# Kernel tuning notes

Measured on AMD Instinct MI355X. Metric: run time of the kernel, lower is better.

The kernel has to match this reference:

```python
import jax, jax.numpy as jnp
import numpy as np

N, E, IN, HID, CLS = 40000, 640000, 128, 256, 40
K = 2  # SGConv k hops

def setup_inputs() -> dict:
    key = jax.random.key(0)
    ks = jax.random.split(key, 5)
    features = jax.random.normal(ks[0], (N, IN), dtype=jnp.float32)
    src = jax.random.randint(ks[1], (E,), 0, N)
    dst = jax.random.randint(ks[2], (E,), 0, N)
    # SGConv fc: in_feats -> n_hidden
    W1 = jax.random.normal(ks[3], (IN, HID), dtype=jnp.float32) / np.float32(np.sqrt(IN))
    b1 = jnp.zeros((HID,), dtype=jnp.float32)
    # model-level linear: n_hidden -> n_classes
    W2 = jax.random.normal(ks[4], (HID, CLS), dtype=jnp.float32) / np.float32(np.sqrt(HID))
    b2 = jnp.zeros((CLS,), dtype=jnp.float32)
    return {"features": features, "src": src, "dst": dst,
            "W1": W1, "b1": b1, "W2": W2, "b2": b2}

def reference(features, src, dst, W1, b1, W2, b2):
    # symmetric degree norm (DGL SGConv: in-degree, clamp min=1)
    deg = jax.ops.segment_sum(jnp.ones((E,), jnp.float32), dst, num_segments=N)
    norm = jax.lax.rsqrt(jnp.maximum(deg, 1.0))[:, None]  # [N,1]
    h = features
    for _ in range(K):
        h = h * norm
        h = jax.ops.segment_sum(h[src], dst, num_segments=N)  # A @ h via edge scatter
        h = h * norm
    h = h @ W1 + b1            # SGConv fc
    return jax.nn.relu(h) @ W2 + b2  # model relu + linear
```

## Files before the change

### kernel.cpp

```cpp
#include <hip/hip_runtime.h>

#define N_NODES 40000
#define N_EDGES 640000
#define IN_F 128
#define HID_F 256
#define CLS_F 40
#define CLS_P 48
#define MB 32
#define TS_LD 264
#define A_LD 136

typedef __attribute__((ext_vector_type(8))) short bf16x8;
typedef __attribute__((ext_vector_type(4))) float f32x4;
typedef __attribute__((ext_vector_type(4))) _Float16 half4;
typedef __attribute__((ext_vector_type(8))) _Float16 half8;

#define MFMA(a, b, c) __builtin_amdgcn_mfma_f32_16x16x32_bf16(a, b, c, 0, 0, 0)

__device__ __forceinline__ unsigned short f32_to_bf16_rne(float f) {
    unsigned int u = __float_as_uint(f);
    unsigned int r = u + 0x7fffu + ((u >> 16) & 1u);
    return (unsigned short)(r >> 16);
}

__device__ __forceinline__ int aswz(int row, int col_us) {
    return row * A_LD + (col_us ^ ((row & 7) << 3));
}


__global__ void k_count(const int* __restrict__ dst, int* __restrict__ counts) {
    int e = blockIdx.x * blockDim.x + threadIdx.x;
    if (e < N_EDGES) atomicAdd(&counts[dst[e]], 1);
}

__global__ void k_scan1(const int* __restrict__ counts, int* __restrict__ bsum) {
    __shared__ int s[256];
    int i = blockIdx.x * 256 + threadIdx.x;
    s[threadIdx.x] = (i < N_NODES) ? counts[i] : 0;
    __syncthreads();
    for (int off = 128; off > 0; off >>= 1) {
        if (threadIdx.x < off) s[threadIdx.x] += s[threadIdx.x + off];
        __syncthreads();
    }
    if (threadIdx.x == 0) bsum[blockIdx.x] = s[0];
}

__global__ void k_scan2(int* __restrict__ bsum, int nb) {
    __shared__ int s[256];
    int t = threadIdx.x;
    int v = (t < nb) ? bsum[t] : 0;
    s[t] = v;
    __syncthreads();
    for (int off = 1; off < 256; off <<= 1) {
        int x = (t >= off) ? s[t - off] : 0;
        __syncthreads();
        s[t] += x;
        __syncthreads();
    }
    if (t < nb) bsum[t] = s[t] - v;
}

__global__ void k_scan3n(const int* __restrict__ counts, const int* __restrict__ bsum,
                         int* __restrict__ rowptr, int* __restrict__ cursor,
                         float* __restrict__ norm, float* __restrict__ norm2) {
    __shared__ int s[256];
    int t = threadIdx.x;
    int i = blockIdx.x * 256 + t;
    int v = (i < N_NODES) ? counts[i] : 0;
    s[t] = v;
    __syncthreads();
    for (int off = 1; off < 256; off <<= 1) {
        int x = (t >= off) ? s[t - off] : 0;
        __syncthreads();
        s[t] += x;
        __syncthreads();
    }
    if (i < N_NODES) {
        int excl = s[t] - v + bsum[blockIdx.x];
        rowptr[i] = excl;
        cursor[i] = excl;
        float d = (float)v;
        float r = rsqrtf(fmaxf(d, 1.0f));
        norm[i] = r;
        norm2[i] = r * r;
    }
}


__global__ __launch_bounds__(256) void k_fsp(
        const int* __restrict__ src, const int* __restrict__ dst,
        int* __restrict__ cursor, unsigned short* __restrict__ csr_src,
        const float* __restrict__ features, const float* __restrict__ norm,
        _Float16* __restrict__ xs,
        const float* __restrict__ W1, const float* __restrict__ W2,
        unsigned short* __restrict__ w1hi, unsigned short* __restrict__ w1lo,
        unsigned short* __restrict__ w2hi, unsigned short* __restrict__ w2lo) {
    int b = blockIdx.x;
    if (b < 2500) {
        int e = b * 256 + threadIdx.x;
        int d = dst[e];
        int p = atomicAdd(&cursor[d], 1);
        csr_src[p] = (unsigned short)src[e];
    } else if (b < 5000) {
        int i = (b - 2500) * 256 + threadIdx.x;
        float s = norm[i >> 4];
        float4 a = ((const float4*)features)[i * 2];
        float4 c = ((const float4*)features)[i * 2 + 1];
        half8 h;
        h[0] = (_Float16)(a.x * s); h[1] = (_Float16)(a.y * s);
        h[2] = (_Float16)(a.z * s); h[3] = (_Float16)(a.w * s);
        h[4] = (_Float16)(c.x * s); h[5] = (_Float16)(c.y * s);
        h[6] = (_Float16)(c.z * s); h[7] = (_Float16)(c.w * s);
        ((half8*)xs)[i] = h;
    } else {
        int idx = (b - 5000) * 256 + threadIdx.x;
        if (idx < IN_F * HID_F) {
            int k = idx >> 8;
            int c = idx & 255;
            float v = W1[idx];
            unsigned short hi = f32_to_bf16_rne(v);
            float fh = __uint_as_float((unsigned)hi << 16);
            w1hi[c * IN_F + k] = hi;
            w1lo[c * IN_F + k] = f32_to_bf16_rne(v - fh);
        }
        int idx2 = idx - IN_F * HID_F;
        if (idx2 >= 0 && idx2 < CLS_P * HID_F) {
            int c = idx2 >> 8;
            int k = idx2 & 255;
            float v = (c < CLS_F) ? W2[k * CLS_F + c] : 0.f;
            unsigned short hi = f32_to_bf16_rne(v);
            float fh = __uint_as_float((unsigned)hi << 16);
            w2hi[c * HID_F + k] = hi;
            w2lo[c * HID_F + k] = f32_to_bf16_rne(v - fh);
        }
    }
}


__global__ __launch_bounds__(256) void k_hop(
        const _Float16* __restrict__ gin, _Float16* __restrict__ gout,
        const unsigned short* __restrict__ csr_src, const int* __restrict__ rowptr,
        const int* __restrict__ counts, const float* __restrict__ oscale) {
    int gid  = blockIdx.x * 8 + (threadIdx.x >> 5);
    int lane = threadIdx.x & 31;
    if (gid >= N_NODES) return;
    int start = rowptr[gid];
    int cnt   = counts[gid];
    const _Float16* base = gin + lane * 4;
    float4 acc = make_float4(0.f, 0.f, 0.f, 0.f);
    int i = 0;
    for (; i + 3 < cnt; i += 4) {
        int s0 = csr_src[start + i];     int s1 = csr_src[start + i + 1];
        int s2 = csr_src[start + i + 2]; int s3 = csr_src[start + i + 3];
        half4 v0 = *(const half4*)(base + (size_t)s0 * IN_F);
        half4 v1 = *(const half4*)(base + (size_t)s1 * IN_F);
        half4 v2 = *(const half4*)(base + (size_t)s2 * IN_F);
        half4 v3 = *(const half4*)(base + (size_t)s3 * IN_F);
        acc.x += (float)v0[0] + (float)v1[0] + (float)v2[0] + (float)v3[0];
        acc.y += (float)v0[1] + (float)v1[1] + (float)v2[1] + (float)v3[1];
        acc.z += (float)v0[2] + (float)v1[2] + (float)v2[2] + (float)v3[2];
        acc.w += (float)v0[3] + (float)v1[3] + (float)v2[3] + (float)v3[3];
    }
    for (; i < cnt; i++) {
        int s = csr_src[start + i];
        half4 v = *(const half4*)(base + (size_t)s * IN_F);
        acc.x += (float)v[0]; acc.y += (float)v[1];
        acc.z += (float)v[2]; acc.w += (float)v[3];
    }
    float sc = oscale[gid];
    half4 o;
    o[0] = (_Float16)(acc.x * sc); o[1] = (_Float16)(acc.y * sc);
    o[2] = (_Float16)(acc.z * sc); o[3] = (_Float16)(acc.w * sc);
    *(half4*)(gout + (size_t)gid * IN_F + lane * 4) = o;
}


__global__ __launch_bounds__(256, 2) void k_mlp(
        const _Float16* __restrict__ h1,
        const unsigned short* __restrict__ csr_src, const int* __restrict__ rowptr,
        const int* __restrict__ counts, const float* __restrict__ norm,
        const unsigned short* __restrict__ w1hi, const unsigned short* __restrict__ w1lo,
        const float* __restrict__ b1,
        const unsigned short* __restrict__ w2hi, const unsigned short* __restrict__ w2lo,
        const float* __restrict__ b2,
        float* __restrict__ out) {
    __shared__ __align__(16) unsigned short ahi[MB * A_LD];
    __shared__ __align__(16) unsigned short alo[MB * A_LD];
    __shared__ __align__(16) unsigned short tshi[MB * TS_LD];
    __shared__ __align__(16) unsigned short tslo[MB * TS_LD];
    int n0 = blockIdx.x * MB;
    int t  = threadIdx.x;
    int w  = t >> 6;
    int l  = t & 63;
    int lr = l & 15;
    int lg = l >> 4;

    bf16x8 b1h[4][4], b1l[4][4];
    float  b1v[4];
    #pragma unroll
    for (int ct = 0; ct < 4; ct++) {
        int col = w * 64 + ct * 16 + lr;
        const unsigned short* bhp = w1hi + (size_t)col * IN_F + lg * 8;
        const unsigned short* blp = w1lo + (size_t)col * IN_F + lg * 8;
        #pragma unroll
        for (int kq = 0; kq < 4; kq++) {
            b1h[ct][kq] = *(const bf16x8*)(bhp + kq * 32);
            b1l[ct][kq] = *(const bf16x8*)(blp + kq * 32);
        }
        b1v[ct] = b1[col];
    }

    {
        int grp  = t >> 5;
        int lane = t & 31;
        for (int nn = grp; nn < MB; nn += 8) {
            int gid = n0 + nn;
            int start = rowptr[gid];
            int cnt   = counts[gid];
            const _Float16* base = h1 + lane * 4;
            float4 acc = make_float4(0.f, 0.f, 0.f, 0.f);
            int i = 0;
            for (; i + 3 < cnt; i += 4) {
                int s0 = csr_src[start + i];     int s1 = csr_src[start + i + 1];
                int s2 = csr_src[start + i + 2]; int s3 = csr_src[start + i + 3];
                half4 v0 = *(const half4*)(base + (size_t)s0 * IN_F);
                half4 v1 = *(const half4*)(base + (size_t)s1 * IN_F);
                half4 v2 = *(const half4*)(base + (size_t)s2 * IN_F);
                half4 v3 = *(const half4*)(base + (size_t)s3 * IN_F);
                acc.x += (float)v0[0] + (float)v1[0] + (float)v2[0] + (float)v3[0];
                acc.y += (float)v0[1] + (float)v1[1] + (float)v2[1] + (float)v3[1];
                acc.z += (float)v0[2] + (float)v1[2] + (float)v2[2] + (float)v3[2];
                acc.w += (float)v0[3] + (float)v1[3] + (float)v2[3] + (float)v3[3];
            }
            for (; i < cnt; i++) {
                int s = csr_src[start + i];
                half4 v = *(const half4*)(base + (size_t)s * IN_F);
                acc.x += (float)v[0]; acc.y += (float)v[1];
                acc.z += (float)v[2]; acc.w += (float)v[3];
            }
            float sc = norm[gid];
            float vv[4] = {acc.x * sc, acc.y * sc, acc.z * sc, acc.w * sc};
            ushort4 h, lo4;
            unsigned short* hp = (unsigned short*)&h;
            unsigned short* lp = (unsigned short*)&lo4;
            #pragma unroll
            for (int j = 0; j < 4; j++) {
                unsigned short hi = f32_to_bf16_rne(vv[j]);
                float fh = __uint_as_float((unsigned)hi << 16);
                hp[j] = hi;
                lp[j] = f32_to_bf16_rne(vv[j] - fh);
            }
            int o = aswz(nn, lane * 4);
            *(ushort4*)&ahi[o] = h;
            *(ushort4*)&alo[o] = lo4;
        }
    }
    __syncthreads();

    #pragma unroll
    for (int rt = 0; rt < 2; rt++) {
        bf16x8 aH[4], aL[4];
        #pragma unroll
        for (int kq = 0; kq < 4; kq++) {
            int o = aswz(rt * 16 + lr, (kq * 4 + lg) * 8);
            aH[kq] = *(const bf16x8*)&ahi[o];
            aL[kq] = *(const bf16x8*)&alo[o];
        }
        #pragma unroll
        for (int ct = 0; ct < 4; ct++) {
            f32x4 acc = {0.f, 0.f, 0.f, 0.f};
            #pragma unroll
            for (int kq = 0; kq < 4; kq++) {
                acc = MFMA(aH[kq], b1h[ct][kq], acc);
                acc = MFMA(aH[kq], b1l[ct][kq], acc);
                acc = MFMA(aL[kq], b1h[ct][kq], acc);
            }
            int col = w * 64 + ct * 16 + lr;
            #pragma unroll
            for (int r = 0; r < 4; r++) {
                int row = rt * 16 + lg * 4 + r;
                float v = acc[r] + b1v[ct];
                v = v > 0.f ? v : 0.f;
                unsigned short hi = f32_to_bf16_rne(v);
                float fh = __uint_as_float((unsigned)hi << 16);
                tshi[row * TS_LD + col] = hi;
                tslo[row * TS_LD + col] = f32_to_bf16_rne(v - fh);
            }
        }
    }
    __syncthreads();

    if (w < 3) {
        int col = w * 16 + lr;
        bf16x8 b2h[8], b2l[8];
        const unsigned short* bhp = w2hi + (size_t)col * HID_F + lg * 8;
        const unsigned short* blp = w2lo + (size_t)col * HID_F + lg * 8;
        #pragma unroll
        for (int kk = 0; kk < 8; kk++) {
            b2h[kk] = *(const bf16x8*)(bhp + kk * 32);
            b2l[kk] = *(const bf16x8*)(blp + kk * 32);
        }
        float bias = (col < CLS_F) ? b2[col] : 0.f;
        #pragma unroll
        for (int rt2 = 0; rt2 < 2; rt2++) {
            const unsigned short* ahp = tshi + (rt2 * 16 + lr) * TS_LD + lg * 8;
            const unsigned short* alp = tslo + (rt2 * 16 + lr) * TS_LD + lg * 8;
            f32x4 acc0 = {0.f, 0.f, 0.f, 0.f};
            f32x4 acc1 = {0.f, 0.f, 0.f, 0.f};
            #pragma unroll
            for (int kk = 0; kk < 4; kk++) {
                bf16x8 a_h0 = *(const bf16x8*)(ahp + kk * 32);
                bf16x8 a_l0 = *(const bf16x8*)(alp + kk * 32);
                bf16x8 a_h1 = *(const bf16x8*)(ahp + (kk + 4) * 32);
                bf16x8 a_l1 = *(const bf16x8*)(alp + (kk + 4) * 32);
                acc0 = MFMA(a_h0, b2h[kk], acc0);
                acc1 = MFMA(a_h1, b2h[kk + 4], acc1);
                acc0 = MFMA(a_h0, b2l[kk], acc0);
                acc1 = MFMA(a_h1, b2l[kk + 4], acc1);
                acc0 = MFMA(a_l0, b2h[kk], acc0);
                acc1 = MFMA(a_l1, b2h[kk + 4], acc1);
            }
            if (col < CLS_F) {
                #pragma unroll
                for (int r = 0; r < 4; r++) {
                    int mrow = n0 + rt2 * 16 + lg * 4 + r;
                    out[(size_t)mrow * CLS_F + col] = acc0[r] + acc1[r] + bias;
                }
            }
        }
    }
}


extern "C" void kernel_launch(void* const* d_in, const int* in_sizes, int n_in,
                              void* d_out, int out_size, void* d_ws, size_t ws_size,
                              hipStream_t stream) {
    const float* features = (const float*)d_in[0];
    const int*   src      = (const int*)d_in[1];
    const int*   dst      = (const int*)d_in[2];
    const float* W1       = (const float*)d_in[3];
    const float* b1       = (const float*)d_in[4];
    const float* W2       = (const float*)d_in[5];
    const float* b2       = (const float*)d_in[6];
    float*       out      = (float*)d_out;

    char* ws = (char*)d_ws;
    size_t off = 0;
    auto alloc = [&](size_t bytes) -> void* {
        void* p = ws + off;
        off += (bytes + 255) & ~(size_t)255;
        return p;
    };
    int*   counts = (int*)alloc((size_t)N_NODES * 4);
    int*   rowptr = (int*)alloc((size_t)N_NODES * 4);
    int*   cursor = (int*)alloc((size_t)N_NODES * 4);
    int*   bsum   = (int*)alloc(256 * 4);
    float* norm   = (float*)alloc((size_t)N_NODES * 4);
    float* norm2  = (float*)alloc((size_t)N_NODES * 4);
    unsigned short* csr = (unsigned short*)alloc((size_t)N_EDGES * 2);
    _Float16* xs  = (_Float16*)alloc((size_t)N_NODES * IN_F * 2);
    _Float16* h1  = (_Float16*)alloc((size_t)N_NODES * IN_F * 2);
    unsigned short* w1hi = (unsigned short*)alloc((size_t)HID_F * IN_F * 2);
    unsigned short* w1lo = (unsigned short*)alloc((size_t)HID_F * IN_F * 2);
    unsigned short* w2hi = (unsigned short*)alloc((size_t)CLS_P * HID_F * 2);
    unsigned short* w2lo = (unsigned short*)alloc((size_t)CLS_P * HID_F * 2);

    hipMemsetAsync(counts, 0, (size_t)N_NODES * 4, stream);

    int nb = (N_NODES + 255) / 256;
    k_count<<<(N_EDGES + 255) / 256, 256, 0, stream>>>(dst, counts);
    k_scan1<<<nb, 256, 0, stream>>>(counts, bsum);
    k_scan2<<<1, 256, 0, stream>>>(bsum, nb);
    k_scan3n<<<nb, 256, 0, stream>>>(counts, bsum, rowptr, cursor, norm, norm2);

    int prep_blocks = (IN_F * HID_F + CLS_P * HID_F + 255) / 256;
    k_fsp<<<5000 + prep_blocks, 256, 0, stream>>>(
        src, dst, cursor, csr, features, norm, xs, W1, W2, w1hi, w1lo, w2hi, w2lo);

    k_hop<<<(N_NODES + 7) / 8, 256, 0, stream>>>(xs, h1, csr, rowptr, counts, norm2);
    k_mlp<<<N_NODES / MB, 256, 0, stream>>>(h1, csr, rowptr, counts, norm,
                                            w1hi, w1lo, b1, w2hi, w2lo, b2, out);
}
```

Before: 262.5 us.

## Switch MLP to fp16 hi/lo MFMA, split second hop out, single-pass scan

Measured after the change: 222.9 us. 15.1% less time.

```diff
diff --git a/kernel.cpp b/kernel.cpp
--- a/kernel.cpp
+++ b/kernel.cpp
@@ -8,62 +8,29 @@
 #define CLS_P 48
 #define MB 32
 #define TS_LD 264
-#define A_LD 136
-
-typedef __attribute__((ext_vector_type(8))) short bf16x8;
+#define LO_SCALE 2048.0f
+#define LO_INV   4.8828125e-4f
+
+typedef __attribute__((ext_vector_type(8))) _Float16 f16x8;
 typedef __attribute__((ext_vector_type(4))) float f32x4;
 typedef __attribute__((ext_vector_type(4))) _Float16 half4;
 typedef __attribute__((ext_vector_type(8))) _Float16 half8;
 
-#define MFMA(a, b, c) __builtin_amdgcn_mfma_f32_16x16x32_bf16(a, b, c, 0, 0, 0)
-
-__device__ __forceinline__ unsigned short f32_to_bf16_rne(float f) {
-    unsigned int u = __float_as_uint(f);
-    unsigned int r = u + 0x7fffu + ((u >> 16) & 1u);
-    return (unsigned short)(r >> 16);
-}
-
-__device__ __forceinline__ int aswz(int row, int col_us) {
-    return row * A_LD + (col_us ^ ((row & 7) << 3));
-}
-
-
-__global__ void k_count(const int* __restrict__ dst, int* __restrict__ counts) {
+#define MFMA16(a, b, c) __builtin_amdgcn_mfma_f32_16x16x32_f16(a, b, c, 0, 0, 0)
+
+
+__global__ void k_count(const int* __restrict__ dst, int* __restrict__ counts,
+                        int* __restrict__ gcur) {
     int e = blockIdx.x * blockDim.x + threadIdx.x;
+    if (e == 0) *gcur = 0;
     if (e < N_EDGES) atomicAdd(&counts[dst[e]], 1);
 }
 
-__global__ void k_scan1(const int* __restrict__ counts, int* __restrict__ bsum) {
+__global__ void k_scanA(const int* __restrict__ counts, int* __restrict__ gcur,
+                        int* __restrict__ rowptr, int* __restrict__ cursor,
+                        float* __restrict__ norm, float* __restrict__ norm2) {
     __shared__ int s[256];
-    int i = blockIdx.x * 256 + threadIdx.x;
-    s[threadIdx.x] = (i < N_NODES) ? counts[i] : 0;
-    __syncthreads();
-    for (int off = 128; off > 0; off >>= 1) {
-        if (threadIdx.x < off) s[threadIdx.x] += s[threadIdx.x + off];
-        __syncthreads();
-    }
-    if (threadIdx.x == 0) bsum[blockIdx.x] = s[0];
-}
-
-__global__ void k_scan2(int* __restrict__ bsum, int nb) {
-    __shared__ int s[256];
-    int t = threadIdx.x;
-    int v = (t < nb) ? bsum[t] : 0;
-    s[t] = v;
-    __syncthreads();
-    for (int off = 1; off < 256; off <<= 1) {
-        int x = (t >= off) ? s[t - off] : 0;
-        __syncthreads();
-        s[t] += x;
-        __syncthreads();
-    }
-    if (t < nb) bsum[t] = s[t] - v;
-}
-
-__global__ void k_scan3n(const int* __restrict__ counts, const int* __restrict__ bsum,
-                         int* __restrict__ rowptr, int* __restrict__ cursor,
-                         float* __restrict__ norm, float* __restrict__ norm2) {
-    __shared__ int s[256];
+    __shared__ int base;
     int t = threadIdx.x;
     int i = blockIdx.x * 256 + t;
     int v = (i < N_NODES) ? counts[i] : 0;
@@ -75,12 +42,13 @@
         s[t] += x;
         __syncthreads();
     }
+    if (t == 255) base = atomicAdd(gcur, s[255]);
+    __syncthreads();
     if (i < N_NODES) {
-        int excl = s[t] - v + bsum[blockIdx.x];
+        int excl = base + s[t] - v;
         rowptr[i] = excl;
         cursor[i] = excl;
-        float d = (float)v;
-        float r = rsqrtf(fmaxf(d, 1.0f));
+        float r = rsqrtf(fmaxf((float)v, 1.0f));
         norm[i] = r;
         norm2[i] = r * r;
     }
@@ -93,8 +61,8 @@
         const float* __restrict__ features, const float* __restrict__ norm,
         _Float16* __restrict__ xs,
         const float* __restrict__ W1, const float* __restrict__ W2,
-        unsigned short* __restrict__ w1hi, unsigned short* __restrict__ w1lo,
-        unsigned short* __restrict__ w2hi, unsigned short* __restrict__ w2lo) {
+        _Float16* __restrict__ w1hi, _Float16* __restrict__ w1lo,
+        _Float16* __restrict__ w2hi, _Float16* __restrict__ w2lo) {
     int b = blockIdx.x;
     if (b < 2500) {
         int e = b * 256 + threadIdx.x;
@@ -118,20 +86,18 @@
             int k = idx >> 8;
             int c = idx & 255;
             float v = W1[idx];
-            unsigned short hi = f32_to_bf16_rne(v);
-            float fh = __uint_as_float((unsigned)hi << 16);
+            _Float16 hi = (_Float16)v;
             w1hi[c * IN_F + k] = hi;
-            w1lo[c * IN_F + k] = f32_to_bf16_rne(v - fh);
+            w1lo[c * IN_F + k] = (_Float16)((v - (float)hi) * LO_SCALE);
         }
         int idx2 = idx - IN_F * HID_F;
         if (idx2 >= 0 && idx2 < CLS_P * HID_F) {
             int c = idx2 >> 8;
             int k = idx2 & 255;
             float v = (c < CLS_F) ? W2[k * CLS_F + c] : 0.f;
-            unsigned short hi = f32_to_bf16_rne(v);
-            float fh = __uint_as_float((unsigned)hi << 16);
+            _Float16 hi = (_Float16)v;
             w2hi[c * HID_F + k] = hi;
-            w2lo[c * HID_F + k] = f32_to_bf16_rne(v - fh);
+            w2lo[c * HID_F + k] = (_Float16)((v - (float)hi) * LO_SCALE);
         }
     }
 }
@@ -176,18 +142,13 @@
 
 
 __global__ __launch_bounds__(256, 2) void k_mlp(
-        const _Float16* __restrict__ h1,
-        const unsigned short* __restrict__ csr_src, const int* __restrict__ rowptr,
-        const int* __restrict__ counts, const float* __restrict__ norm,
-        const unsigned short* __restrict__ w1hi, const unsigned short* __restrict__ w1lo,
+        const _Float16* __restrict__ h2,
+        const _Float16* __restrict__ w1hi, const _Float16* __restrict__ w1lo,
         const float* __restrict__ b1,
-        const unsigned short* __restrict__ w2hi, const unsigned short* __restrict__ w2lo,
+        const _Float16* __restrict__ w2hi, const _Float16* __restrict__ w2lo,
         const float* __restrict__ b2,
         float* __restrict__ out) {
-    __shared__ __align__(16) unsigned short ahi[MB * A_LD];
-    __shared__ __align__(16) unsigned short alo[MB * A_LD];
-    __shared__ __align__(16) unsigned short tshi[MB * TS_LD];
-    __shared__ __align__(16) unsigned short tslo[MB * TS_LD];
+    __shared__ __align__(16) _Float16 ts[MB * TS_LD];
     int n0 = blockIdx.x * MB;
     int t  = threadIdx.x;
     int w  = t >> 6;
@@ -195,96 +156,49 @@
     int lr = l & 15;
     int lg = l >> 4;
 
-    bf16x8 b1h[4][4], b1l[4][4];
-    float  b1v[4];
+    f16x8 b1h[4][4], b1l[4][4];
+    float b1v[4];
     #pragma unroll
     for (int ct = 0; ct < 4; ct++) {
         int col = w * 64 + ct * 16 + lr;
-        const unsigned short* bhp = w1hi + (size_t)col * IN_F + lg * 8;
-        const unsigned short* blp = w1lo + (size_t)col * IN_F + lg * 8;
+        const _Float16* bhp = w1hi + (size_t)col * IN_F + lg * 8;
+        const _Float16* blp = w1lo + (size_t)col * IN_F + lg * 8;
         #pragma unroll
         for (int kq = 0; kq < 4; kq++) {
-            b1h[ct][kq] = *(const bf16x8*)(bhp + kq * 32);
-            b1l[ct][kq] = *(const bf16x8*)(blp + kq * 32);
+            b1h[ct][kq] = *(const f16x8*)(bhp + kq * 32);
+            b1l[ct][kq] = *(const f16x8*)(blp + kq * 32);
         }
         b1v[ct] = b1[col];
     }
 
+    f16x8 aA[4], aB[4];
     {
-        int grp  = t >> 5;
-        int lane = t & 31;
-        for (int nn = grp; nn < MB; nn += 8) {
-            int gid = n0 + nn;
-            int start = rowptr[gid];
-            int cnt   = counts[gid];
-            const _Float16* base = h1 + lane * 4;
-            float4 acc = make_float4(0.f, 0.f, 0.f, 0.f);
-            int i = 0;
-            for (; i + 3 < cnt; i += 4) {
-                int s0 = csr_src[start + i];     int s1 = csr_src[start + i + 1];
-                int s2 = csr_src[start + i + 2]; int s3 = csr_src[start + i + 3];
-                half4 v0 = *(const half4*)(base + (size_t)s0 * IN_F);
-                half4 v1 = *(const half4*)(base + (size_t)s1 * IN_F);
-                half4 v2 = *(const half4*)(base + (size_t)s2 * IN_F);
-                half4 v3 = *(const half4*)(base + (size_t)s3 * IN_F);
-                acc.x += (float)v0[0] + (float)v1[0] + (float)v2[0] + (float)v3[0];
-                acc.y += (float)v0[1] + (float)v1[1] + (float)v2[1] + (float)v3[1];
-                acc.z += (float)v0[2] + (float)v1[2] + (float)v2[2] + (float)v3[2];
-                acc.w += (float)v0[3] + (float)v1[3] + (float)v2[3] + (float)v3[3];
-            }
-            for (; i < cnt; i++) {
-                int s = csr_src[start + i];
-                half4 v = *(const half4*)(base + (size_t)s * IN_F);
-                acc.x += (float)v[0]; acc.y += (float)v[1];
-                acc.z += (float)v[2]; acc.w += (float)v[3];
-            }
-            float sc = norm[gid];
-            float vv[4] = {acc.x * sc, acc.y * sc, acc.z * sc, acc.w * sc};
-            ushort4 h, lo4;
-            unsigned short* hp = (unsigned short*)&h;
-            unsigned short* lp = (unsigned short*)&lo4;
-            #pragma unroll
-            for (int j = 0; j < 4; j++) {
-                unsigned short hi = f32_to_bf16_rne(vv[j]);
-                float fh = __uint_as_float((unsigned)hi << 16);
-                hp[j] = hi;
-                lp[j] = f32_to_bf16_rne(vv[j] - fh);
-            }
-            int o = aswz(nn, lane * 4);
-            *(ushort4*)&ahi[o] = h;
-            *(ushort4*)&alo[o] = lo4;
-        }
-    }
-    __syncthreads();
-
+        const _Float16* pa = h2 + (size_t)(n0 + lr) * IN_F + lg * 8;
+        const _Float16* pb = h2 + (size_t)(n0 + 16 + lr) * IN_F + lg * 8;
+        #pragma unroll
+        for (int kq = 0; kq < 4; kq++) {
+            aA[kq] = *(const f16x8*)(pa + kq * 32);
+            aB[kq] = *(const f16x8*)(pb + kq * 32);
+        }
+    }
     #pragma unroll
     for (int rt = 0; rt < 2; rt++) {
-        bf16x8 aH[4], aL[4];
-        #pragma unroll
-        for (int kq = 0; kq < 4; kq++) {
-            int o = aswz(rt * 16 + lr, (kq * 4 + lg) * 8);
-            aH[kq] = *(const bf16x8*)&ahi[o];
-            aL[kq] = *(const bf16x8*)&alo[o];
-        }
         #pragma unroll
         for (int ct = 0; ct < 4; ct++) {
-            f32x4 acc = {0.f, 0.f, 0.f, 0.f};
+            f32x4 acch = {0.f, 0.f, 0.f, 0.f};
+            f32x4 accl = {0.f, 0.f, 0.f, 0.f};
             #pragma unroll
             for (int kq = 0; kq < 4; kq++) {
-                acc = MFMA(aH[kq], b1h[ct][kq], acc);
-                acc = MFMA(aH[kq], b1l[ct][kq], acc);
-                acc = MFMA(aL[kq], b1h[ct][kq], acc);
+                f16x8 a = rt == 0 ? aA[kq] : aB[kq];
+                acch = MFMA16(a, b1h[ct][kq], acch);
+                accl = MFMA16(a, b1l[ct][kq], accl);
             }
             int col = w * 64 + ct * 16 + lr;
             #pragma unroll
             for (int r = 0; r < 4; r++) {
                 int row = rt * 16 + lg * 4 + r;
-                float v = acc[r] + b1v[ct];
-                v = v > 0.f ? v : 0.f;
-                unsigned short hi = f32_to_bf16_rne(v);
-                float fh = __uint_as_float((unsigned)hi << 16);
-                tshi[row * TS_LD + col] = hi;
-                tslo[row * TS_LD + col] = f32_to_bf16_rne(v - fh);
+                float v = acch[r] + accl[r] * LO_INV + b1v[ct];
+                ts[row * TS_LD + col] = (_Float16)(v > 0.f ? v : 0.f);
             }
         }
     }
@@ -292,39 +206,37 @@
 
     if (w < 3) {
         int col = w * 16 + lr;
-        bf16x8 b2h[8], b2l[8];
-        const unsigned short* bhp = w2hi + (size_t)col * HID_F + lg * 8;
-        const unsigned short* blp = w2lo + (size_t)col * HID_F + lg * 8;
+        f16x8 b2h[8], b2l[8];
+        const _Float16* bhp = w2hi + (size_t)col * HID_F + lg * 8;
+        const _Float16* blp = w2lo + (size_t)col * HID_F + lg * 8;
         #pragma unroll
         for (int kk = 0; kk < 8; kk++) {
-            b2h[kk] = *(const bf16x8*)(bhp + kk * 32);
-            b2l[kk] = *(const bf16x8*)(blp + kk * 32);
+            b2h[kk] = *(const f16x8*)(bhp + kk * 32);
+            b2l[kk] = *(const f16x8*)(blp + kk * 32);
         }
         float bias = (col < CLS_F) ? b2[col] : 0.f;
         #pragma unroll
         for (int rt2 = 0; rt2 < 2; rt2++) {
-            const unsigned short* ahp = tshi + (rt2 * 16 + lr) * TS_LD + lg * 8;
-            const unsigned short* alp = tslo + (rt2 * 16 + lr) * TS_LD + lg * 8;
-            f32x4 acc0 = {0.f, 0.f, 0.f, 0.f};
-            f32x4 acc1 = {0.f, 0.f, 0.f, 0.f};
+            const _Float16* ahp = ts + (rt2 * 16 + lr) * TS_LD + lg * 8;
+            f32x4 acch0 = {0.f, 0.f, 0.f, 0.f};
+            f32x4 acch1 = {0.f, 0.f, 0.f, 0.f};
+            f32x4 accl0 = {0.f, 0.f, 0.f, 0.f};
+            f32x4 accl1 = {0.f, 0.f, 0.f, 0.f};
             #pragma unroll
             for (int kk = 0; kk < 4; kk++) {
-                bf16x8 a_h0 = *(const bf16x8*)(ahp + kk * 32);
-                bf16x8 a_l0 = *(const bf16x8*)(alp + kk * 32);
-                bf16x8 a_h1 = *(const bf16x8*)(ahp + (kk + 4) * 32);
-                bf16x8 a_l1 = *(const bf16x8*)(alp + (kk + 4) * 32);
-                acc0 = MFMA(a_h0, b2h[kk], acc0);
-                acc1 = MFMA(a_h1, b2h[kk + 4], acc1);
-                acc0 = MFMA(a_h0, b2l[kk], acc0);
-                acc1 = MFMA(a_h1, b2l[kk + 4], acc1);
-                acc0 = MFMA(a_l0, b2h[kk], acc0);
-                acc1 = MFMA(a_l1, b2h[kk + 4], acc1);
+                f16x8 a0 = *(const f16x8*)(ahp + kk * 32);
+                f16x8 a1 = *(const f16x8*)(ahp + (kk + 4) * 32);
+                acch0 = MFMA16(a0, b2h[kk], acch0);
+                acch1 = MFMA16(a1, b2h[kk + 4], acch1);
+                accl0 = MFMA16(a0, b2l[kk], accl0);
+                accl1 = MFMA16(a1, b2l[kk + 4], accl1);
             }
             if (col < CLS_F) {
                 #pragma unroll
                 for (int r = 0; r < 4; r++) {
                     int mrow = n0 + rt2 * 16 + lg * 4 + r;
-                    out[(size_t)mrow * CLS_F + col] = acc0[r] + acc1[r] + bias;
+                    out[(size_t)mrow * CLS_F + col] =
+                        (acch0[r] + acch1[r]) + (accl0[r] + accl1[r]) * LO_INV + bias;
                 }
             }
         }
@@ -352,32 +264,32 @@
         return p;
     };
     int*   counts = (int*)alloc((size_t)N_NODES * 4);
+    int*   gcur   = (int*)alloc(256);
     int*   rowptr = (int*)alloc((size_t)N_NODES * 4);
     int*   cursor = (int*)alloc((size_t)N_NODES * 4);
-    int*   bsum   = (int*)alloc(256 * 4);
     float* norm   = (float*)alloc((size_t)N_NODES * 4);
     float* norm2  = (float*)alloc((size_t)N_NODES * 4);
     unsigned short* csr = (unsigned short*)alloc((size_t)N_EDGES * 2);
     _Float16* xs  = (_Float16*)alloc((size_t)N_NODES * IN_F * 2);
     _Float16* h1  = (_Float16*)alloc((size_t)N_NODES * IN_F * 2);
-    unsigned short* w1hi = (unsigned short*)alloc((size_t)HID_F * IN_F * 2);
-    unsigned short* w1lo = (unsigned short*)alloc((size_t)HID_F * IN_F * 2);
-    unsigned short* w2hi = (unsigned short*)alloc((size_t)CLS_P * HID_F * 2);
-    unsigned short* w2lo = (unsigned short*)alloc((size_t)CLS_P * HID_F * 2);
+    _Float16* h2  = (_Float16*)alloc((size_t)N_NODES * IN_F * 2);
+    _Float16* w1hi = (_Float16*)alloc((size_t)HID_F * IN_F * 2);
+    _Float16* w1lo = (_Float16*)alloc((size_t)HID_F * IN_F * 2);
+    _Float16* w2hi = (_Float16*)alloc((size_t)CLS_P * HID_F * 2);
+    _Float16* w2lo = (_Float16*)alloc((size_t)CLS_P * HID_F * 2);
 
     hipMemsetAsync(counts, 0, (size_t)N_NODES * 4, stream);
 
     int nb = (N_NODES + 255) / 256;
-    k_count<<<(N_EDGES + 255) / 256, 256, 0, stream>>>(dst, counts);
-    k_scan1<<<nb, 256, 0, stream>>>(counts, bsum);
-    k_scan2<<<1, 256, 0, stream>>>(bsum, nb);
-    k_scan3n<<<nb, 256, 0, stream>>>(counts, bsum, rowptr, cursor, norm, norm2);
+    k_count<<<(N_EDGES + 255) / 256, 256, 0, stream>>>(dst, counts, gcur);
+    k_scanA<<<nb, 256, 0, stream>>>(counts, gcur, rowptr, cursor, norm, norm2);
 
     int prep_blocks = (IN_F * HID_F + CLS_P * HID_F + 255) / 256;
     k_fsp<<<5000 + prep_blocks, 256, 0, stream>>>(
         src, dst, cursor, csr, features, norm, xs, W1, W2, w1hi, w1lo, w2hi, w2lo);
 
     k_hop<<<(N_NODES + 7) / 8, 256, 0, stream>>>(xs, h1, csr, rowptr, counts, norm2);
-    k_mlp<<<N_NODES / MB, 256, 0, stream>>>(h1, csr, rowptr, counts, norm,
-                                            w1hi, w1lo, b1, w2hi, w2lo, b2, out);
-}
+    k_hop<<<(N_NODES + 7) / 8, 256, 0, stream>>>(h1, h2, csr, rowptr, counts, norm);
+
+    k_mlp<<<N_NODES / MB, 256, 0, stream>>>(h2, w1hi, w1lo, b1, w2hi, w2lo, b2, out);
+}
```
